# Kernel tuning notes

Measured on AMD Instinct MI355X. Metric: run time of the kernel, lower is better.

Reference implementation:

```python
import jax, jax.numpy as jnp
import numpy as np

N_NODES = 50000
N_EDGES = 800000
NEG_SLOPE = 0.2


def _gat_layer(x, src, dst, W, a_src, a_dst, bias, heads, out_ch):
    """PyG-style GATConv with self-loops already appended to src/dst."""
    N = x.shape[0]
    h = (x @ W.T).reshape(N, heads, out_ch)            # [N,H,C]
    alpha_src = jnp.einsum('nhc,hc->nh', h, a_src)      # [N,H]
    alpha_dst = jnp.einsum('nhc,hc->nh', h, a_dst)      # [N,H]
    e = jax.nn.leaky_relu(alpha_src[src] + alpha_dst[dst], NEG_SLOPE)  # [E,H]
    # segment softmax over incoming edges of each destination node
    m = jax.ops.segment_max(e, dst, num_segments=N)     # [N,H]
    ex = jnp.exp(e - m[dst])
    denom = jax.ops.segment_sum(ex, dst, num_segments=N)  # [N,H] (>0: self-loops)
    alpha = ex / (denom[dst] + 1e-16)                    # [E,H]
    out = jax.ops.segment_sum(h[src] * alpha[:, :, None], dst, num_segments=N)  # [N,H,C]
    return out.reshape(N, heads * out_ch) + bias


def _with_self_loops(edge_index, n):
    loop = jnp.arange(n, dtype=edge_index.dtype)
    src = jnp.concatenate([edge_index[0], loop])
    dst = jnp.concatenate([edge_index[1], loop])
    return src, dst


def setup_inputs() -> dict:
    key = jax.random.key(0)
    ks = jax.random.split(key, 12)
    s = lambda fan: 1.0 / np.sqrt(fan)
    return {
        'x': jax.random.normal(ks[0], (N_NODES, 16), jnp.float32),
        'edge_index': jax.random.randint(ks[1], (2, N_EDGES), 0, N_NODES, jnp.int64),
        'W1': jax.random.normal(ks[2], (256, 16), jnp.float32) * s(16),
        'att_src1': jax.random.normal(ks[3], (4, 64), jnp.float32) * s(64),
        'att_dst1': jax.random.normal(ks[4], (4, 64), jnp.float32) * s(64),
        'b1': jnp.zeros((256,), jnp.float32),
        'W2': jax.random.normal(ks[5], (64, 256), jnp.float32) * s(256),
        'att_src2': jax.random.normal(ks[6], (1, 64), jnp.float32) * s(64),
        'att_dst2': jax.random.normal(ks[7], (1, 64), jnp.float32) * s(64),
        'b2': jnp.zeros((64,), jnp.float32),
        'fc_w': jax.random.normal(ks[8], (1, 64), jnp.float32) * s(64),
        'fc_b': jnp.zeros((1,), jnp.float32),
    }


def reference(x, edge_index, W1, att_src1, att_dst1, b1,
              W2, att_src2, att_dst2, b2, fc_w, fc_b):
    src, dst = _with_self_loops(edge_index, x.shape[0])
    h = jax.nn.elu(_gat_layer(x, src, dst, W1, att_src1, att_dst1, b1, heads=4, out_ch=64))
    h = jax.nn.elu(_gat_layer(h, src, dst, W2, att_src2, att_dst2, b2, heads=1, out_ch=64))
    return h @ fc_w.T + fc_b
```

## Files before the change

### kernel.cpp

```cpp
#include <hip/hip_runtime.h>
#include <hip/hip_bf16.h>
#include <stdint.h>

#define N_NODES 50000
#define N_EDGES 800000
#define MAXDEG  96
#define NSLICE  6250
#define NSB     196

#define OFF_X    0
#define OFF_W1   800000
#define OFF_AS1  804096
#define OFF_AD1  804352
#define OFF_B1   804608
#define OFF_W2   804864
#define OFF_AS2  821248
#define OFF_AD2  821312
#define OFF_B2   821376
#define OFF_FCW  821440
#define OFF_FCB  821504
#define N_CANON  821505
#define N_W2B    16384
#define N_W1B    16384
#define N_CONV   (N_CANON + N_W2B + N_W1B + N_NODES)

#define TSTRIDE 264

typedef __hip_bfloat16 bf16;
typedef __attribute__((ext_vector_type(8))) short short8;
typedef __attribute__((ext_vector_type(4))) float f32x4;

__device__ __forceinline__ float b2f(bf16 v){ return (float)v; }
__device__ __forceinline__ int clampi(int v, int lo, int hi){ return v < lo ? lo : (v > hi ? hi : v); }
__device__ __forceinline__ float clampf(float v){ return fminf(fmaxf(v, -40.f), 40.f); }
__device__ __forceinline__ uint16_t f2bfbits(float f){
  union { float f; uint32_t u; } c; c.f = f;
  uint32_t r = c.u + 0x7fff + ((c.u >> 16) & 1);
  return (uint16_t)(r >> 16);
}
__device__ __forceinline__ float bitsf(uint32_t u){
  union { uint32_t u; float f; } c; c.u = u; return c.f;
}
__device__ __forceinline__ uint32_t fbits(float f){
  union { float f; uint32_t u; } c; c.f = f; return c.u;
}

__device__ __forceinline__ int load_src(const int* ei, int i, int f){
  return f ? ei[2*(size_t)i] : ei[i];
}
__device__ __forceinline__ int load_dst(const int* ei, int i, int f){
  return f ? ei[2*((size_t)N_EDGES + i)] : ei[N_EDGES + i];
}

__global__ void k_detect(const int* __restrict__ ei, const uint16_t* __restrict__ xu,
                         int* __restrict__ flag){
  const int l = threadIdx.x;
  int or_odd = ei[2*l + 1] | ei[2*(400000 + l) + 1];
  int hits = 0;
  for(int k = 0; k < 64; k++){
    int e = (xu[l*64 + k] >> 7) & 0xFF;
    hits += (e >= 200);
  }
  #pragma unroll
  for(int off=32; off; off>>=1){
    or_odd |= __shfl_xor(or_odd, off, 64);
    hits   += __shfl_xor(hits,   off, 64);
  }
  if(l == 0){
    flag[0] = (or_odd == 0) ? 1 : 0;
    flag[1] = (hits > 16) ? 1 : 0;
  }
}

__global__ void k_convert(const void* x, const void* W1, const void* as1w, const void* ad1w,
                          const void* b1, const void* W2, const void* as2w, const void* ad2w,
                          const void* b2, const void* fcw, const void* fcb,
                          float* __restrict__ canon, uint16_t* __restrict__ W2b,
                          uint16_t* __restrict__ W1b, int* __restrict__ cnt,
                          int* __restrict__ csr_pad, const int* __restrict__ flag){
  int i = blockIdx.x*256 + threadIdx.x;
  int fp32 = flag[1];
  if(i >= N_CANON + N_W2B + N_W1B){
    int j = i - (N_CANON + N_W2B + N_W1B);
    if(j < N_NODES){ cnt[j] = 1; csr_pad[(size_t)j*MAXDEG] = j; }
    return;
  }
  if(i >= N_CANON + N_W2B){
    int j2 = i - (N_CANON + N_W2B);
    int j = j2 >> 6, kk = j2 & 63;
    uint16_t v = 0;
    if((kk >> 4) == (j >> 6)){
      int e = j*16 + (kk & 15);
      v = fp32 ? f2bfbits(((const float*)W1)[e]) : ((const uint16_t*)W1)[e];
    }
    W1b[j2] = v;
    return;
  }
  if(i >= N_CANON){
    int j = i - N_CANON;
    W2b[j] = fp32 ? f2bfbits(((const float*)W2)[j]) : ((const uint16_t*)W2)[j];
    return;
  }
  const void* src; int off;
  if     (i < OFF_W1 ){ src = x;    off = i; }
  else if(i < OFF_AS1){ src = W1;   off = i - OFF_W1; }
  else if(i < OFF_AD1){ src = as1w; off = i - OFF_AS1; }
  else if(i < OFF_B1 ){ src = ad1w; off = i - OFF_AD1; }
  else if(i < OFF_W2 ){ src = b1;   off = i - OFF_B1; }
  else if(i < OFF_AS2){ src = W2;   off = i - OFF_W2; }
  else if(i < OFF_AD2){ src = as2w; off = i - OFF_AS2; }
  else if(i < OFF_B2 ){ src = ad2w; off = i - OFF_AD2; }
  else if(i < OFF_FCW){ src = b2;   off = i - OFF_B2; }
  else if(i < OFF_FCB){ src = fcw;  off = i - OFF_FCW; }
  else               { src = fcb;  off = 0; }
  float v = fp32 ? ((const float*)src)[off] : b2f(((const bf16*)src)[off]);
  canon[i] = v;
}


__global__ __launch_bounds__(256) void k_prepscat(const float* __restrict__ canon,
                        uint32_t* __restrict__ pack, float* __restrict__ dpack,
                        const int* __restrict__ ei, int* __restrict__ cnt,
                        int* __restrict__ csr_pad, const int* __restrict__ flag){
  const int tid = threadIdx.x;
  if(blockIdx.x >= 196){
    const int bid = blockIdx.x - 196;
    const int grp = bid & 7, sb = bid >> 3;
    const int f = flag[0];
    const int lo = grp*NSLICE, hi = lo + NSLICE;
    const int base = sb*4096;
    #pragma unroll 4
    for(int j = 0; j < 16; j++){
      int i = base + j*256 + tid;
      if(i >= N_EDGES) break;
      int d = clampi(load_dst(ei, i, f), 0, N_NODES-1);
      if(d >= lo && d < hi){
        int s = clampi(load_src(ei, i, f), 0, N_NODES-1);
        int pos = atomicAdd(&cnt[d], 1);
        pos = clampi(pos, 0, MAXDEG-1);
        csr_pad[(size_t)d*MAXDEG + pos] = s;
      }
    }
    return;
  }
  __shared__ float ps[64], pd[64];
  if(tid < 128){
    int e = tid & 63;
    int h = e >> 4, k = e & 15;
    const float* av = canon + (tid < 64 ? OFF_AS1 : OFF_AD1) + h*64;
    const float* Wp = canon + OFF_W1 + (h*64)*16 + k;
    float acc = 0.f;
    #pragma unroll 8
    for(int c = 0; c < 64; c++) acc += av[c] * Wp[c*16];
    (tid < 64 ? ps : pd)[e] = acc;
  }
  __syncthreads();
  int n = blockIdx.x*256 + tid;
  if(n >= N_NODES) return;
  float xr[16];
  const float4* xp = (const float4*)(canon + OFF_X + n*16);
  #pragma unroll
  for(int t=0;t<4;t++){ float4 v = xp[t]; xr[4*t]=v.x; xr[4*t+1]=v.y; xr[4*t+2]=v.z; xr[4*t+3]=v.w; }
  uint32_t w[16];
  #pragma unroll
  for(int t=0;t<8;t++)
    w[t] = (uint32_t)f2bfbits(xr[2*t]) | ((uint32_t)f2bfbits(xr[2*t+1]) << 16);
  float qs[8];
  #pragma unroll
  for(int h=0;h<4;h++){
    float a=0.f, b=0.f;
    #pragma unroll
    for(int k=0;k<16;k++){ a += ps[h*16+k]*xr[k]; b += pd[h*16+k]*xr[k]; }
    a = clampf(a); b = clampf(b);
    w[8+2*h]  = fbits(__expf(a));
    w[9+2*h]  = fbits(__expf(0.2f*a));
    qs[2*h]   = __expf(b);
    qs[2*h+1] = __expf(0.2f*b);
  }
  uint4* dst = (uint4*)(pack + (size_t)n*16);
  dst[0] = make_uint4(w[0],w[1],w[2],w[3]);
  dst[1] = make_uint4(w[4],w[5],w[6],w[7]);
  dst[2] = make_uint4(w[8],w[9],w[10],w[11]);
  dst[3] = make_uint4(w[12],w[13],w[14],w[15]);
  float4* dd = (float4*)(dpack + (size_t)n*8);
  dd[0] = make_float4(qs[0],qs[1],qs[2],qs[3]);
  dd[1] = make_float4(qs[4],qs[5],qs[6],qs[7]);
}


struct Acc { float y0,y1,y2,y3,d0,d1,d2,d3; };

__device__ __forceinline__ void batch8(const int* __restrict__ csr, int i0, const char* pk,
                                       float2 qq, int g, int k, int h3, int base, Acc& a){
  int iA = csr[i0 + g], iB = csr[i0 + 4 + g];
  const char* rA = pk + (size_t)iA*64;
  const char* rB = pk + (size_t)iB*64;
  float xvA = bitsf((uint32_t)(*(const uint16_t*)(rA + k*2)) << 16);
  float2 ppA = *(const float2*)(rA + 32 + h3*8);
  float xvB = bitsf((uint32_t)(*(const uint16_t*)(rB + k*2)) << 16);
  float2 ppB = *(const float2*)(rB + 32 + h3*8);
  float wA = fmaxf(ppA.x*qq.x, ppA.y*qq.y);
  float wB = fmaxf(ppB.x*qq.x, ppB.y*qq.y);
  float a0 = __shfl(wA, base|0, 64), a1 = __shfl(wA, base|1, 64);
  float a2 = __shfl(wA, base|2, 64), a3 = __shfl(wA, base|3, 64);
  float b0 = __shfl(wB, base|0, 64), b1 = __shfl(wB, base|1, 64);
  float b2 = __shfl(wB, base|2, 64), b3 = __shfl(wB, base|3, 64);
  a.y0 += a0*xvA + b0*xvB; a.d0 += a0 + b0;
  a.y1 += a1*xvA + b1*xvB; a.d1 += a1 + b1;
  a.y2 += a2*xvA + b2*xvB; a.d2 += a2 + b2;
  a.y3 += a3*xvA + b3*xvB; a.d3 += a3 + b3;
}

__device__ __forceinline__ void tail8(const int* __restrict__ csr, int i0, int end, const char* pk,
                                      float2 qq, int g, int k, int h3, int base, Acc& a){
  int iiA = i0 + g, iiB = i0 + 4 + g;
  bool vA = iiA < end, vB = iiB < end;
  int iA = csr[vA ? iiA : end-1];
  int iB = csr[vB ? iiB : end-1];
  const char* rA = pk + (size_t)iA*64;
  const char* rB = pk + (size_t)iB*64;
  float xvA = bitsf((uint32_t)(*(const uint16_t*)(rA + k*2)) << 16);
  float2 ppA = *(const float2*)(rA + 32 + h3*8);
  float xvB = bitsf((uint32_t)(*(const uint16_t*)(rB + k*2)) << 16);
  float2 ppB = *(const float2*)(rB + 32 + h3*8);
  float wA = vA ? fmaxf(ppA.x*qq.x, ppA.y*qq.y) : 0.f;
  float wB = vB ? fmaxf(ppB.x*qq.x, ppB.y*qq.y) : 0.f;
  float a0 = __shfl(wA, base|0, 64), a1 = __shfl(wA, base|1, 64);
  float a2 = __shfl(wA, base|2, 64), a3 = __shfl(wA, base|3, 64);
  float b0 = __shfl(wB, base|0, 64), b1 = __shfl(wB, base|1, 64);
  float b2 = __shfl(wB, base|2, 64), b3 = __shfl(wB, base|3, 64);
  a.y0 += a0*xvA + b0*xvB; a.d0 += a0 + b0;
  a.y1 += a1*xvA + b1*xvB; a.d1 += a1 + b1;
  a.y2 += a2*xvA + b2*xvB; a.d2 += a2 + b2;
  a.y3 += a3*xvA + b3*xvB; a.d3 += a3 + b3;
}

__device__ __forceinline__ void store_y(Acc& a, int n, int g, int k, uint16_t* __restrict__ yb){
  a.y0 += __shfl_xor(a.y0,16,64); a.y0 += __shfl_xor(a.y0,32,64);
  a.y1 += __shfl_xor(a.y1,16,64); a.y1 += __shfl_xor(a.y1,32,64);
  a.y2 += __shfl_xor(a.y2,16,64); a.y2 += __shfl_xor(a.y2,32,64);
  a.y3 += __shfl_xor(a.y3,16,64); a.y3 += __shfl_xor(a.y3,32,64);
  a.d0 += __shfl_xor(a.d0,16,64); a.d0 += __shfl_xor(a.d0,32,64);
  a.d1 += __shfl_xor(a.d1,16,64); a.d1 += __shfl_xor(a.d1,32,64);
  a.d2 += __shfl_xor(a.d2,16,64); a.d2 += __shfl_xor(a.d2,32,64);
  a.d3 += __shfl_xor(a.d3,16,64); a.d3 += __shfl_xor(a.d3,32,64);
  float yH = (g==0) ? a.y0 : (g==1) ? a.y1 : (g==2) ? a.y2 : a.y3;
  float dH = (g==0) ? a.d0 : (g==1) ? a.d1 : (g==2) ? a.d2 : a.d3;
  yb[(size_t)n*64 + g*16 + k] = f2bfbits(yH / (dH + 1e-16f));
}

__global__ __launch_bounds__(256) void k_aggy(const int* __restrict__ cnt, const int* __restrict__ csr_pad,
                       const uint32_t* __restrict__ pack, const float* __restrict__ dpack,
                       uint16_t* __restrict__ yb){
  const int wv = threadIdx.x >> 6, lane = threadIdx.x & 63;
  const int g = lane >> 4, k = lane & 15, h3 = k & 3;
  const int base = lane & 48;
  const char* pk = (const char*)pack;

  for(int np = blockIdx.x*4 + wv; np < N_NODES/2; np += gridDim.x*4){
    const int nA = np*2, nB = np*2 + 1;
    const int begA = nA*MAXDEG, endA = begA + cnt[nA];
    const int begB = nB*MAXDEG, endB = begB + cnt[nB];
    const float2 qqA = *(const float2*)(dpack + (size_t)nA*8 + h3*2);
    const float2 qqB = *(const float2*)(dpack + (size_t)nB*8 + h3*2);
    Acc aA = {0,0,0,0,0,0,0,0}, aB = {0,0,0,0,0,0,0,0};
    int iA = begA, iB = begB;
    while(iA + 8 <= endA && iB + 8 <= endB){
      batch8(csr_pad, iA, pk, qqA, g, k, h3, base, aA);
      batch8(csr_pad, iB, pk, qqB, g, k, h3, base, aB);
      iA += 8; iB += 8;
    }
    while(iA + 8 <= endA){ batch8(csr_pad, iA, pk, qqA, g, k, h3, base, aA); iA += 8; }
    while(iB + 8 <= endB){ batch8(csr_pad, iB, pk, qqB, g, k, h3, base, aB); iB += 8; }
    if(iA < endA) tail8(csr_pad, iA, endA, pk, qqA, g, k, h3, base, aA);
    if(iB < endB) tail8(csr_pad, iB, endB, pk, qqB, g, k, h3, base, aB);
    store_y(aA, nA, g, k, yb);
    store_y(aB, nB, g, k, yb);
  }
}


__global__ __launch_bounds__(256) void k_mlp(const uint16_t* __restrict__ yb,
                        const uint16_t* __restrict__ W1b, const uint16_t* __restrict__ W2b,
                        const float* __restrict__ canon,
                        bf16* __restrict__ h2, float2* __restrict__ pq2, float2* __restrict__ dq2){
  __shared__ uint16_t w1lds[N_W1B];
  __shared__ uint16_t tile[4][16*TSTRIDE];
  const int tid = threadIdx.x, lane = tid & 63, wave = tid >> 6;
  const int quad = lane >> 4, c = lane & 15;

  {
    const uint4* src = (const uint4*)W1b;
    uint4* dst = (uint4*)w1lds;
    for(int idx = tid; idx < N_W1B/8; idx += 256) dst[idx] = src[idx];
  }
  __syncthreads();

  short8 bfrag[4][8];
  #pragma unroll
  for(int cb=0; cb<4; cb++)
    #pragma unroll
    for(int ks=0; ks<8; ks++)
      bfrag[cb][ks] = *(const short8*)(W2b + (cb*16 + c)*256 + ks*32 + quad*8);

  float b1v[16];
  #pragma unroll
  for(int cb=0; cb<16; cb++) b1v[cb] = canon[OFF_B1 + cb*16 + c];
  float asj[4], adj[4];
  #pragma unroll
  for(int cb=0; cb<4; cb++){
    asj[cb] = canon[OFF_AS2 + cb*16 + c];
    adj[cb] = canon[OFF_AD2 + cb*16 + c];
  }

  uint16_t* tl = tile[wave];
  const int tiles = N_NODES/16;
  const int gw = blockIdx.x*4 + wave, nw = gridDim.x*4;
  for(int t = gw; t < tiles; t += nw){
    const int n0 = t*16;
    short8 af0 = *(const short8*)(yb + (size_t)(n0 + c)*64 + quad*8);
    short8 af1 = *(const short8*)(yb + (size_t)(n0 + c)*64 + 32 + quad*8);
    #pragma unroll
    for(int cb=0; cb<16; cb++){
      short8 wf = *(const short8*)(w1lds + (cb*16 + c)*64 + (cb>>3)*32 + quad*8);
      f32x4 acc = (f32x4){0.f,0.f,0.f,0.f};
      acc = __builtin_amdgcn_mfma_f32_16x16x32_bf16((cb>>3) ? af1 : af0, wf, acc, 0,0,0);
      #pragma unroll
      for(int r=0; r<4; r++){
        float o = acc[r] + b1v[cb];
        o = (o > 0.f) ? o : expm1f(o);
        tl[(quad*4 + r)*TSTRIDE + cb*16 + c] = f2bfbits(o);
      }
    }
    f32x4 acc2[4];
    #pragma unroll
    for(int cb=0; cb<4; cb++) acc2[cb] = (f32x4){0.f,0.f,0.f,0.f};
    #pragma unroll
    for(int ks=0; ks<8; ks++){
      short8 af = *(const short8*)(tl + c*TSTRIDE + ks*32 + quad*8);
      acc2[0] = __builtin_amdgcn_mfma_f32_16x16x32_bf16(af, bfrag[0][ks], acc2[0], 0,0,0);
      acc2[1] = __builtin_amdgcn_mfma_f32_16x16x32_bf16(af, bfrag[1][ks], acc2[1], 0,0,0);
      acc2[2] = __builtin_amdgcn_mfma_f32_16x16x32_bf16(af, bfrag[2][ks], acc2[2], 0,0,0);
      acc2[3] = __builtin_amdgcn_mfma_f32_16x16x32_bf16(af, bfrag[3][ks], acc2[3], 0,0,0);
    }
    float vs[4] = {0.f,0.f,0.f,0.f}, vd[4] = {0.f,0.f,0.f,0.f};
    #pragma unroll
    for(int cb=0; cb<4; cb++)
      #pragma unroll
      for(int r=0; r<4; r++){
        float v = acc2[cb][r];
        h2[(size_t)(n0 + quad*4 + r)*64 + cb*16 + c] = __float2bfloat16(v);
        vs[r] += v * asj[cb];
        vd[r] += v * adj[cb];
      }
    #pragma unroll
    for(int r=0; r<4; r++){
      #pragma unroll
      for(int off=1; off<16; off<<=1){
        vs[r] += __shfl_xor(vs[r], off, 64);
        vd[r] += __shfl_xor(vd[r], off, 64);
      }
    }
    if(c == 0){
      #pragma unroll
      for(int r=0; r<4; r++){
        float s = clampf(vs[r]), d = clampf(vd[r]);
        pq2[n0 + quad*4 + r] = make_float2(__expf(s), __expf(0.2f*s));
        dq2[n0 + quad*4 + r] = make_float2(__expf(d), __expf(0.2f*d));
      }
    }
  }
}


__global__ __launch_bounds__(256) void k_agg2(const int* __restrict__ cnt, const int* __restrict__ csr_pad,
                       const bf16* __restrict__ h2, const float2* __restrict__ pq2,
                       const float2* __restrict__ dq2, const float* __restrict__ canon,
                       void* __restrict__ outv, const int* __restrict__ flag){
  const int wv = threadIdx.x >> 6, lane = threadIdx.x & 63;
  const int g = lane >> 4, k = lane & 15;
  const char* h2b = (const char*)h2;
  float4 b2v = ((const float4*)(canon + OFF_B2))[k];
  float4 fcv = ((const float4*)(canon + OFF_FCW))[k];
  const float fcb0 = canon[OFF_FCB];
  const int ofp32 = flag[1];
  for(int n = blockIdx.x*4 + wv; n < N_NODES; n += gridDim.x*4){
    const int beg = n*MAXDEG, end = beg + cnt[n];
    const float2 qn = dq2[n];
    float a0=0.f,a1=0.f,a2=0.f,a3=0.f, den=0.f;
    int i0 = beg;
    const int nfull = (end - beg) >> 3;
    if(nfull > 0){
      int iA = csr_pad[i0 + g], iB = csr_pad[i0 + 4 + g];
      for(int b = 1; b < nfull; b++){
        int nA = csr_pad[i0 + 8 + g], nB = csr_pad[i0 + 12 + g];
        uint2 hA = *(const uint2*)(h2b + (size_t)iA*128 + k*8);
        float2 pA = pq2[iA];
        uint2 hB = *(const uint2*)(h2b + (size_t)iB*128 + k*8);
        float2 pB = pq2[iB];
        float wA = fmaxf(pA.x*qn.x, pA.y*qn.y);
        float wB = fmaxf(pB.x*qn.x, pB.y*qn.y);
        den += wA + wB;
        a0 += wA*bitsf(hA.x << 16) + wB*bitsf(hB.x << 16);
        a1 += wA*bitsf(hA.x & 0xffff0000u) + wB*bitsf(hB.x & 0xffff0000u);
        a2 += wA*bitsf(hA.y << 16) + wB*bitsf(hB.y << 16);
        a3 += wA*bitsf(hA.y & 0xffff0000u) + wB*bitsf(hB.y & 0xffff0000u);
        iA = nA; iB = nB;
        i0 += 8;
      }
      {
        uint2 hA = *(const uint2*)(h2b + (size_t)iA*128 + k*8);
        float2 pA = pq2[iA];
        uint2 hB = *(const uint2*)(h2b + (size_t)iB*128 + k*8);
        float2 pB = pq2[iB];
        float wA = fmaxf(pA.x*qn.x, pA.y*qn.y);
        float wB = fmaxf(pB.x*qn.x, pB.y*qn.y);
        den += wA + wB;
        a0 += wA*bitsf(hA.x << 16) + wB*bitsf(hB.x << 16);
        a1 += wA*bitsf(hA.x & 0xffff0000u) + wB*bitsf(hB.x & 0xffff0000u);
        a2 += wA*bitsf(hA.y << 16) + wB*bitsf(hB.y << 16);
        a3 += wA*bitsf(hA.y & 0xffff0000u) + wB*bitsf(hB.y & 0xffff0000u);
        i0 += 8;
      }
    }
    if(i0 < end){
      int iiA = i0 + g, iiB = i0 + 4 + g;
      bool vA = iiA < end, vB = iiB < end;
      int iA = csr_pad[vA ? iiA : end-1];
      int iB = csr_pad[vB ? iiB : end-1];
      uint2 hA = *(const uint2*)(h2b + (size_t)iA*128 + k*8);
      float2 pA = pq2[iA];
      uint2 hB = *(const uint2*)(h2b + (size_t)iB*128 + k*8);
      float2 pB = pq2[iB];
      float wA = vA ? fmaxf(pA.x*qn.x, pA.y*qn.y) : 0.f;
      float wB = vB ? fmaxf(pB.x*qn.x, pB.y*qn.y) : 0.f;
      den += wA + wB;
      a0 += wA*bitsf(hA.x << 16) + wB*bitsf(hB.x << 16);
      a1 += wA*bitsf(hA.x & 0xffff0000u) + wB*bitsf(hB.x & 0xffff0000u);
      a2 += wA*bitsf(hA.y << 16) + wB*bitsf(hB.y << 16);
      a3 += wA*bitsf(hA.y & 0xffff0000u) + wB*bitsf(hB.y & 0xffff0000u);
    }
    a0 += __shfl_xor(a0,16,64); a0 += __shfl_xor(a0,32,64);
    a1 += __shfl_xor(a1,16,64); a1 += __shfl_xor(a1,32,64);
    a2 += __shfl_xor(a2,16,64); a2 += __shfl_xor(a2,32,64);
    a3 += __shfl_xor(a3,16,64); a3 += __shfl_xor(a3,32,64);
    den += __shfl_xor(den,16,64); den += __shfl_xor(den,32,64);
    float inv = 1.f/(den + 1e-16f);
    float o0 = a0*inv + b2v.x, o1 = a1*inv + b2v.y;
    float o2 = a2*inv + b2v.z, o3 = a3*inv + b2v.w;
    o0 = (o0>0.f)?o0:expm1f(o0); o1 = (o1>0.f)?o1:expm1f(o1);
    o2 = (o2>0.f)?o2:expm1f(o2); o3 = (o3>0.f)?o3:expm1f(o3);
    float v = o0*fcv.x + o1*fcv.y + o2*fcv.z + o3*fcv.w;
    v += __shfl_xor(v,1,64); v += __shfl_xor(v,2,64);
    v += __shfl_xor(v,4,64); v += __shfl_xor(v,8,64);
    if(lane == 0){
      float r = v + fcb0;
      if(ofp32) ((float*)outv)[n] = r;
      else      ((bf16*)outv)[n] = __float2bfloat16(r);
    }
  }
}


extern "C" void kernel_launch(void* const* d_in, const int* in_sizes, int n_in,
                              void* d_out, int out_size, void* d_ws, size_t ws_size,
                              hipStream_t stream){
  (void)in_sizes; (void)n_in; (void)out_size;
  const int* ei = (const int*)d_in[1];

  char* w = (char*)d_ws;
  auto carve = [&](size_t bytes)->char*{ char* p = w; w += (bytes + 255) & ~(size_t)255; return p; };
  int*      cnt     = (int*)     carve((size_t)N_NODES*4);
  int*      flag    = (int*)     carve(256);
  int*      csr_pad = (int*)     carve((size_t)N_NODES*MAXDEG*4);
  float*    canon   = (float*)   carve((size_t)N_CANON*4);
  uint16_t* W2b     = (uint16_t*)carve((size_t)N_W2B*2);
  uint16_t* W1b     = (uint16_t*)carve((size_t)N_W1B*2);
  uint32_t* pack    = (uint32_t*)carve((size_t)N_NODES*64);
  float*    dpack   = (float*)   carve((size_t)N_NODES*32);
  uint16_t* yb      = (uint16_t*)carve((size_t)N_NODES*64*2);
  float2*   pq2     = (float2*)  carve((size_t)N_NODES*8);
  float2*   dq2     = (float2*)  carve((size_t)N_NODES*8);
  bf16*     h2      = (bf16*)    carve((size_t)N_NODES*64*2);
  size_t required = (size_t)(w - (char*)d_ws);
  if(ws_size < required) return;

  hipLaunchKernelGGL(k_detect,   dim3(1), dim3(64), 0, stream, ei, (const uint16_t*)d_in[0], flag);
  hipLaunchKernelGGL(k_convert,  dim3((N_CONV+255)/256), dim3(256), 0, stream,
                     d_in[0], d_in[2], d_in[3], d_in[4], d_in[5], d_in[6], d_in[7], d_in[8],
                     d_in[9], d_in[10], d_in[11], canon, W2b, W1b, cnt, csr_pad, flag);
  hipLaunchKernelGGL(k_prepscat, dim3(196 + 8*NSB), dim3(256), 0, stream,
                     canon, pack, dpack, ei, cnt, csr_pad, flag);
  hipLaunchKernelGGL(k_aggy,     dim3(2048), dim3(256), 0, stream, cnt, csr_pad, pack, dpack, yb);
  hipLaunchKernelGGL(k_mlp,      dim3(782), dim3(256), 0, stream, yb, W1b, W2b, canon, h2, pq2, dq2);
  hipLaunchKernelGGL(k_agg2,     dim3(2048), dim3(256), 0, stream, cnt, csr_pad, h2, pq2, dq2, canon, d_out, flag);
}
```

Before: 212.0 us.

## Restructure MLP kernel to one wave per 16-node tile, drop LDS weight staging

The fused MLP kernel now launches one 64-thread block per 16-node tile instead of persistent 256-thread blocks looping over tiles. W1 is no longer staged into LDS, and W2 fragments are no longer held in registers; both are read from global memory (via cache) inside the MFMA loops, which lowers LDS and register pressure so more waves can be resident. ELU also switches from expm1f to __expf(o)-1. The risk is repeated global and L2 weight reads per tile and slightly lower ELU precision near zero.

```diff
diff --git a/kernel.cpp b/kernel.cpp
--- a/kernel.cpp
+++ b/kernel.cpp
@@ -280,28 +280,14 @@
 }
 
 
-__global__ __launch_bounds__(256) void k_mlp(const uint16_t* __restrict__ yb,
+__global__ __launch_bounds__(64, 4) void k_mlp(const uint16_t* __restrict__ yb,
                         const uint16_t* __restrict__ W1b, const uint16_t* __restrict__ W2b,
                         const float* __restrict__ canon,
                         bf16* __restrict__ h2, float2* __restrict__ pq2, float2* __restrict__ dq2){
-  __shared__ uint16_t w1lds[N_W1B];
-  __shared__ uint16_t tile[4][16*TSTRIDE];
-  const int tid = threadIdx.x, lane = tid & 63, wave = tid >> 6;
+  __shared__ uint16_t tl[16*TSTRIDE];
+  const int lane = threadIdx.x & 63;
   const int quad = lane >> 4, c = lane & 15;
-
-  {
-    const uint4* src = (const uint4*)W1b;
-    uint4* dst = (uint4*)w1lds;
-    for(int idx = tid; idx < N_W1B/8; idx += 256) dst[idx] = src[idx];
-  }
-  __syncthreads();
-
-  short8 bfrag[4][8];
-  #pragma unroll
-  for(int cb=0; cb<4; cb++)
-    #pragma unroll
-    for(int ks=0; ks<8; ks++)
-      bfrag[cb][ks] = *(const short8*)(W2b + (cb*16 + c)*256 + ks*32 + quad*8);
+  const int n0 = blockIdx.x * 16;
 
   float b1v[16];
   #pragma unroll
@@ -313,61 +299,56 @@
     adj[cb] = canon[OFF_AD2 + cb*16 + c];
   }
 
-  uint16_t* tl = tile[wave];
-  const int tiles = N_NODES/16;
-  const int gw = blockIdx.x*4 + wave, nw = gridDim.x*4;
-  for(int t = gw; t < tiles; t += nw){
-    const int n0 = t*16;
-    short8 af0 = *(const short8*)(yb + (size_t)(n0 + c)*64 + quad*8);
-    short8 af1 = *(const short8*)(yb + (size_t)(n0 + c)*64 + 32 + quad*8);
-    #pragma unroll
-    for(int cb=0; cb<16; cb++){
-      short8 wf = *(const short8*)(w1lds + (cb*16 + c)*64 + (cb>>3)*32 + quad*8);
-      f32x4 acc = (f32x4){0.f,0.f,0.f,0.f};
-      acc = __builtin_amdgcn_mfma_f32_16x16x32_bf16((cb>>3) ? af1 : af0, wf, acc, 0,0,0);
-      #pragma unroll
-      for(int r=0; r<4; r++){
-        float o = acc[r] + b1v[cb];
-        o = (o > 0.f) ? o : expm1f(o);
-        tl[(quad*4 + r)*TSTRIDE + cb*16 + c] = f2bfbits(o);
-      }
-    }
-    f32x4 acc2[4];
-    #pragma unroll
-    for(int cb=0; cb<4; cb++) acc2[cb] = (f32x4){0.f,0.f,0.f,0.f};
-    #pragma unroll
-    for(int ks=0; ks<8; ks++){
-      short8 af = *(const short8*)(tl + c*TSTRIDE + ks*32 + quad*8);
-      acc2[0] = __builtin_amdgcn_mfma_f32_16x16x32_bf16(af, bfrag[0][ks], acc2[0], 0,0,0);
-      acc2[1] = __builtin_amdgcn_mfma_f32_16x16x32_bf16(af, bfrag[1][ks], acc2[1], 0,0,0);
-      acc2[2] = __builtin_amdgcn_mfma_f32_16x16x32_bf16(af, bfrag[2][ks], acc2[2], 0,0,0);
-      acc2[3] = __builtin_amdgcn_mfma_f32_16x16x32_bf16(af, bfrag[3][ks], acc2[3], 0,0,0);
-    }
-    float vs[4] = {0.f,0.f,0.f,0.f}, vd[4] = {0.f,0.f,0.f,0.f};
-    #pragma unroll
-    for(int cb=0; cb<4; cb++)
-      #pragma unroll
-      for(int r=0; r<4; r++){
-        float v = acc2[cb][r];
-        h2[(size_t)(n0 + quad*4 + r)*64 + cb*16 + c] = __float2bfloat16(v);
-        vs[r] += v * asj[cb];
-        vd[r] += v * adj[cb];
-      }
+  short8 af0 = *(const short8*)(yb + (size_t)(n0 + c)*64 + quad*8);
+  short8 af1 = *(const short8*)(yb + (size_t)(n0 + c)*64 + 32 + quad*8);
+  #pragma unroll
+  for(int cb=0; cb<16; cb++){
+    short8 wf = *(const short8*)(W1b + (cb*16 + c)*64 + (cb>>3)*32 + quad*8);
+    f32x4 acc = (f32x4){0.f,0.f,0.f,0.f};
+    acc = __builtin_amdgcn_mfma_f32_16x16x32_bf16((cb>>3) ? af1 : af0, wf, acc, 0,0,0);
     #pragma unroll
     for(int r=0; r<4; r++){
-      #pragma unroll
-      for(int off=1; off<16; off<<=1){
-        vs[r] += __shfl_xor(vs[r], off, 64);
-        vd[r] += __shfl_xor(vd[r], off, 64);
-      }
-    }
-    if(c == 0){
-      #pragma unroll
-      for(int r=0; r<4; r++){
-        float s = clampf(vs[r]), d = clampf(vd[r]);
-        pq2[n0 + quad*4 + r] = make_float2(__expf(s), __expf(0.2f*s));
-        dq2[n0 + quad*4 + r] = make_float2(__expf(d), __expf(0.2f*d));
-      }
+      float o = acc[r] + b1v[cb];
+      o = (o > 0.f) ? o : (__expf(o) - 1.f);
+      tl[(quad*4 + r)*TSTRIDE + cb*16 + c] = f2bfbits(o);
+    }
+  }
+  f32x4 acc2[4];
+  #pragma unroll
+  for(int cb=0; cb<4; cb++) acc2[cb] = (f32x4){0.f,0.f,0.f,0.f};
+  #pragma unroll
+  for(int ks=0; ks<8; ks++){
+    short8 af = *(const short8*)(tl + c*TSTRIDE + ks*32 + quad*8);
+    #pragma unroll
+    for(int cb=0; cb<4; cb++){
+      short8 bfrag = *(const short8*)(W2b + (cb*16 + c)*256 + ks*32 + quad*8);
+      acc2[cb] = __builtin_amdgcn_mfma_f32_16x16x32_bf16(af, bfrag, acc2[cb], 0,0,0);
+    }
+  }
+  float vs[4] = {0.f,0.f,0.f,0.f}, vd[4] = {0.f,0.f,0.f,0.f};
+  #pragma unroll
+  for(int cb=0; cb<4; cb++)
+    #pragma unroll
+    for(int r=0; r<4; r++){
+      float v = acc2[cb][r];
+      h2[(size_t)(n0 + quad*4 + r)*64 + cb*16 + c] = __float2bfloat16(v);
+      vs[r] += v * asj[cb];
+      vd[r] += v * adj[cb];
+    }
+  #pragma unroll
+  for(int r=0; r<4; r++){
+    #pragma unroll
+    for(int off=1; off<16; off<<=1){
+      vs[r] += __shfl_xor(vs[r], off, 64);
+      vd[r] += __shfl_xor(vd[r], off, 64);
+    }
+  }
+  if(c == 0){
+    #pragma unroll
+    for(int r=0; r<4; r++){
+      float s = clampf(vs[r]), d = clampf(vd[r]);
+      pq2[n0 + quad*4 + r] = make_float2(__expf(s), __expf(0.2f*s));
+      dq2[n0 + quad*4 + r] = make_float2(__expf(d), __expf(0.2f*d));
     }
   }
 }
@@ -492,6 +473,6 @@
   hipLaunchKernelGGL(k_prepscat, dim3(196 + 8*NSB), dim3(256), 0, stream,
                      canon, pack, dpack, ei, cnt, csr_pad, flag);
   hipLaunchKernelGGL(k_aggy,     dim3(2048), dim3(256), 0, stream, cnt, csr_pad, pack, dpack, yb);
-  hipLaunchKernelGGL(k_mlp,      dim3(782), dim3(256), 0, stream, yb, W1b, W2b, canon, h2, pq2, dq2);
+  hipLaunchKernelGGL(k_mlp,      dim3(N_NODES/16), dim3(64), 0, stream, yb, W1b, W2b, canon, h2, pq2, dq2);
   hipLaunchKernelGGL(k_agg2,     dim3(2048), dim3(256), 0, stream, cnt, csr_pad, h2, pq2, dq2, canon, d_out, flag);
 }
```

After: 201.8 us. 4.8% less time.
